# Performance work log

Hardware: AMD Instinct MI355X
Metric: run time of the kernel (lower is better)

## Reference

```python
import jax, jax.numpy as jnp
import numpy as np
import math

MIN_NORM = 1e-15
EPS = 4e-3  # float32 boundary eps used by PoincareBall.proj
C = 1.0


def artanh(x):
    x = jnp.clip(x, -1.0 + 1e-7, 1.0 - 1e-7)
    return 0.5 * (jnp.log1p(x) - jnp.log1p(-x))


def _norm(x):
    return jnp.maximum(jnp.linalg.norm(x, axis=-1, keepdims=True), MIN_NORM)


def proj(x, c):
    n = _norm(x)
    maxnorm = (1.0 - EPS) / jnp.sqrt(c)
    return jnp.where(n > maxnorm, x / n * maxnorm, x)


def expmap0(u, c):
    sc = jnp.sqrt(c)
    n = _norm(u)
    return jnp.tanh(sc * n) * u / (sc * n)


def logmap0(p, c):
    sc = jnp.sqrt(c)
    n = _norm(p)
    return artanh(sc * n) * p / (sc * n)


def mobius_add(x, y, c):
    x2 = jnp.sum(x * x, -1, keepdims=True)
    y2 = jnp.sum(y * y, -1, keepdims=True)
    xy = jnp.sum(x * y, -1, keepdims=True)
    num = (1 + 2 * c * xy + c * y2) * x + (1 - c * x2) * y
    den = 1 + 2 * c * xy + c * c * x2 * y2
    return num / jnp.maximum(den, MIN_NORM)


def mobius_matvec(m, x, c):
    sc = jnp.sqrt(c)
    xn = _norm(x)
    mx = x @ m.T
    mxn = _norm(mx)
    res = jnp.tanh(mxn / xn * artanh(sc * xn)) * mx / (mxn * sc)
    zero = jnp.all(mx == 0, axis=-1, keepdims=True)
    return jnp.where(zero, jnp.zeros((), x.dtype), res)


def hnn_layer(x, W, b, c):
    # HypLinear (dropout=0, use_bias=1) followed by HypAct(relu); proj_tan0 is identity for PoincareBall.
    res = proj(mobius_matvec(W, x, c), c)
    hb = proj(expmap0(b.reshape(1, -1), c), c)
    res = proj(mobius_add(res, hb, c), c)
    xt = jax.nn.relu(logmap0(res, c))
    return proj(expmap0(xt, c), c)


def setup_inputs():
    key = jax.random.key(0)
    ks = jax.random.split(key, 5)
    B, N, K, D = 4, 2000, 5, 32
    H1, H2 = 160, 32  # H_layer1: 32 -> 32*5, H_layer2: 32 -> 32
    # points on the Poincare ball (small norm so logmap0 is well-conditioned)
    in_feats = 0.05 * jax.random.normal(ks[0], (B, N, D), jnp.float32)
    # one-hot neighbor adjacency [batch, agent, nei, agent]
    nei_idx = jax.random.randint(ks[1], (B, N, K), 0, N)
    in_nei = jax.nn.one_hot(nei_idx, N, dtype=jnp.float32)
    # xavier_uniform with gain sqrt(2), zero bias (reset_parameters)
    b1w = math.sqrt(2.0) * math.sqrt(6.0 / (H1 + D))
    b2w = math.sqrt(2.0) * math.sqrt(6.0 / (H2 + H2))
    W1 = jax.random.uniform(ks[2], (H1, D), jnp.float32, -b1w, b1w)
    W2 = jax.random.uniform(ks[3], (H2, H2), jnp.float32, -b2w, b2w)
    b1 = jnp.zeros((H1,), jnp.float32)
    b2 = jnp.zeros((H2,), jnp.float32)
    return {"in_feats": in_feats, "in_nei": in_nei, "W1": W1, "b1": b1,
            "W2": W2, "b2": b2, "h_dim": 32, "head": 5}


def reference(in_feats, in_nei, W1, b1, W2, b2, h_dim, head):
    c = C
    B, N, D = in_feats.shape
    K = in_nei.shape[2]
    # tangent-space features (proj_tan0 is identity)
    feats = logmap0(in_feats, c)                                   # [B,N,D]
    agent = proj(expmap0(feats[:, :, None, :], c), c)              # [B,N,1,D]
    # one-hot adjacency gather: equals matmul(in_nei, repeat(feats)) in the torch code
    nbr_t = jnp.einsum('bnkm,bmd->bnkd', in_nei, feats)            # [B,N,K,D]
    nbr = proj(expmap0(nbr_t, c), c)
    # query heads
    q = logmap0(hnn_layer(agent, W1, b1, c), c)                    # [B,N,1,h*head]
    q = q.reshape(B, N, 1, h_dim, head).transpose(0, 1, 4, 2, 3)   # [B,N,head,1,h]
    # key heads; the torch code recomputes H_layer1(neighbor_repr) for values with
    # identical weights/inputs (dropout=0), so values == keys and we reuse them.
    kv = logmap0(hnn_layer(nbr, W1, b1, c), c)
    kv = kv.reshape(B, N, K, h_dim, head).transpose(0, 1, 4, 2, 3)  # [B,N,head,K,h]
    att = jax.nn.softmax(jnp.einsum('bnhqd,bnhkd->bnhqk', q, kv), axis=-1)  # [B,N,head,1,K]
    att_record = att.reshape(B, N, head, K)
    out = jnp.einsum('bnhqk,bnhkd->bnhqd', att, kv).mean(axis=2)   # [B,N,1,h]
    out = out.reshape(B, N, h_dim)
    out = proj(expmap0(out, c), c)
    out = hnn_layer(out, W2, b2, c)                                # [B,N,32]
    return out, att_record
```

## Files before the change

kernel.cpp:

```cpp
#include <hip/hip_runtime.h>
#include <math.h>

#define BB 4
#define NN 2000
#define KK 5
#define DD 32
#define H1 160
#define HEAD 5
#define HDIM 32
#define MAXNORM 0.996f
#define MINN 1e-15f

#define NIDX_BLOCKS 10000
#define NG_BLOCKS 2000

__device__ __forceinline__ float artanh_f(float x) {
    x = fminf(fmaxf(x, -1.0f + 1e-7f), 1.0f - 1e-7f);
    return 0.5f * (log1pf(x) - log1pf(-x));
}

__device__ __forceinline__ float wave_sum(float v) {
#pragma unroll
    for (int o = 32; o > 0; o >>= 1) v += __shfl_xor(v, o, 64);
    return v;
}

__device__ __forceinline__ float wave_sum32(float v) {
#pragma unroll
    for (int o = 16; o > 0; o >>= 1) v += __shfl_xor(v, o, 64);
    return v;
}

__device__ __forceinline__ void do_find_idx(const float* __restrict__ nei,
                                            int* __restrict__ idx,
                                            int wave, int lane) {
    const float* row = nei + (size_t)wave * NN;
#pragma unroll 1
    for (int it = 0; it < 8; ++it) {
        int base = it * 256 + lane * 4;
        bool found = false;
        int pos = 0;
        if (base < NN) {
            float4 v = *(const float4*)(row + base);
            if (v.x > 0.5f) { found = true; pos = base; }
            if (v.y > 0.5f) { found = true; pos = base + 1; }
            if (v.z > 0.5f) { found = true; pos = base + 2; }
            if (v.w > 0.5f) { found = true; pos = base + 3; }
        }
        unsigned long long m = __ballot(found);
        if (m) {
            if (found) idx[wave] = pos;
            break;
        }
    }
}

__device__ __forceinline__ void do_g(const float* __restrict__ xin,
                                     const float* __restrict__ W1,
                                     const float* __restrict__ b1,
                                     float* __restrict__ g,
                                     int wave, int lane) {
    bool j2ok = lane < (H1 - 128);

    float x = (lane < DD) ? xin[wave * DD + lane] : 0.f;

    float n = fmaxf(sqrtf(wave_sum(x * x)), MINN);
    float f = (artanh_f(n) / n) * x;
    float fn = fmaxf(sqrtf(wave_sum(f * f)), MINN);
    float p = (tanhf(fn) / fn) * f;
    float pn = fmaxf(sqrtf(wave_sum(p * p)), MINN);
    if (pn > MAXNORM) p *= MAXNORM / pn;
    float xn = fmaxf(sqrtf(wave_sum(p * p)), MINN);

    float mx0 = 0.f, mx1 = 0.f, mx2 = 0.f;
#pragma unroll
    for (int d = 0; d < DD; ++d) {
        float pd = __shfl(p, d, 64);
        mx0 += W1[lane * DD + d] * pd;
        mx1 += W1[(lane + 64) * DD + d] * pd;
        if (j2ok) mx2 += W1[(lane + 128) * DD + d] * pd;
    }
    float m2 = mx0 * mx0 + mx1 * mx1 + (j2ok ? mx2 * mx2 : 0.f);
    float mxn = fmaxf(sqrtf(wave_sum(m2)), MINN);
    float sc = tanhf(mxn / xn * artanh_f(xn)) / mxn;
    float r0 = sc * mx0, r1 = sc * mx1, r2 = sc * mx2;
    float rn = fmaxf(sqrtf(wave_sum(r0 * r0 + r1 * r1 + (j2ok ? r2 * r2 : 0.f))), MINN);
    if (rn > MAXNORM) { float s = MAXNORM / rn; r0 *= s; r1 *= s; r2 *= s; }

    float bb0 = b1[lane], bb1 = b1[lane + 64], bb2 = j2ok ? b1[lane + 128] : 0.f;
    float bn = fmaxf(sqrtf(wave_sum(bb0 * bb0 + bb1 * bb1 + bb2 * bb2)), MINN);
    float bs = tanhf(bn) / bn;
    float h0 = bs * bb0, h1 = bs * bb1, h2 = bs * bb2;
    float hn = fmaxf(sqrtf(wave_sum(h0 * h0 + h1 * h1 + h2 * h2)), MINN);
    if (hn > MAXNORM) { float s = MAXNORM / hn; h0 *= s; h1 *= s; h2 *= s; }

    float x2s = wave_sum(r0 * r0 + r1 * r1 + (j2ok ? r2 * r2 : 0.f));
    float y2s = wave_sum(h0 * h0 + h1 * h1 + h2 * h2);
    float xys = wave_sum(r0 * h0 + r1 * h1 + (j2ok ? r2 * h2 : 0.f));
    float ca = 1.f + 2.f * xys + y2s;
    float cb = 1.f - x2s;
    float den = fmaxf(1.f + 2.f * xys + x2s * y2s, MINN);
    float a0 = (ca * r0 + cb * h0) / den;
    float a1 = (ca * r1 + cb * h1) / den;
    float a2 = (ca * r2 + cb * h2) / den;
    float an = fmaxf(sqrtf(wave_sum(a0 * a0 + a1 * a1 + (j2ok ? a2 * a2 : 0.f))), MINN);
    if (an > MAXNORM) { float s = MAXNORM / an; a0 *= s; a1 *= s; a2 *= s; }

    float ln = fmaxf(sqrtf(wave_sum(a0 * a0 + a1 * a1 + (j2ok ? a2 * a2 : 0.f))), MINN);
    float ls = artanh_f(ln) / ln;
    float t0 = fmaxf(ls * a0, 0.f), t1 = fmaxf(ls * a1, 0.f), t2 = fmaxf(ls * a2, 0.f);
    float tn = fmaxf(sqrtf(wave_sum(t0 * t0 + t1 * t1 + (j2ok ? t2 * t2 : 0.f))), MINN);
    float es = tanhf(tn) / tn;
    float y0 = es * t0, y1 = es * t1, y2 = es * t2;
    float yn = fmaxf(sqrtf(wave_sum(y0 * y0 + y1 * y1 + (j2ok ? y2 * y2 : 0.f))), MINN);
    if (yn > MAXNORM) { float s = MAXNORM / yn; y0 *= s; y1 *= s; y2 *= s; }
    float gn = fmaxf(sqrtf(wave_sum(y0 * y0 + y1 * y1 + (j2ok ? y2 * y2 : 0.f))), MINN);
    float gs = artanh_f(gn) / gn;

    float* go = g + (size_t)wave * H1;
    go[lane] = gs * y0;
    go[lane + 64] = gs * y1;
    if (j2ok) go[lane + 128] = gs * y2;
}

__global__ __launch_bounds__(256) void scan_and_g_kernel(const float* __restrict__ nei,
                                                         int* __restrict__ idx,
                                                         const float* __restrict__ xin,
                                                         const float* __restrict__ W1,
                                                         const float* __restrict__ b1,
                                                         float* __restrict__ g) {
    int lane = threadIdx.x & 63;
    int waveInBlock = threadIdx.x >> 6;
    if (blockIdx.x < NIDX_BLOCKS) {
        int wave = blockIdx.x * 4 + waveInBlock;
        do_find_idx(nei, idx, wave, lane);
    } else {
        int wave = (blockIdx.x - NIDX_BLOCKS) * 4 + waveInBlock;
        do_g(xin, W1, b1, g, wave, lane);
    }
}

__global__ __launch_bounds__(256) void fused_att_out_kernel(const float* __restrict__ g,
                                                            const int* __restrict__ idx,
                                                            const float* __restrict__ W2,
                                                            const float* __restrict__ b2,
                                                            float* __restrict__ out,
                                                            float* __restrict__ att_out) {
    int wave = (blockIdx.x * blockDim.x + threadIdx.x) >> 6;
    int lane = threadIdx.x & 63;
    if (wave >= BB * NN) return;
    int r = wave;
    int b = r / NN;
    int d = lane & 31;

    const float* gq = g + (size_t)r * H1;
    float q[HEAD];
#pragma unroll
    for (int h = 0; h < HEAD; ++h) q[h] = gq[d * HEAD + h];

    float kv[KK][HEAD];
    float s[KK][HEAD];
#pragma unroll
    for (int k = 0; k < KK; ++k) {
        int m = idx[r * KK + k];
        const float* gk = g + (size_t)(b * NN + m) * H1;
#pragma unroll
        for (int h = 0; h < HEAD; ++h) kv[k][h] = gk[d * HEAD + h];
#pragma unroll
        for (int h = 0; h < HEAD; ++h) s[k][h] = wave_sum32(q[h] * kv[k][h]);
    }

    float att[HEAD][KK];
#pragma unroll
    for (int h = 0; h < HEAD; ++h) {
        float mxv = s[0][h];
#pragma unroll
        for (int k = 1; k < KK; ++k) mxv = fmaxf(mxv, s[k][h]);
        float sum = 0.f;
#pragma unroll
        for (int k = 0; k < KK; ++k) { att[h][k] = expf(s[k][h] - mxv); sum += att[h][k]; }
        float inv = 1.f / sum;
#pragma unroll
        for (int k = 0; k < KK; ++k) att[h][k] *= inv;
    }
    if (lane < HEAD * KK) {
        int h = lane / KK, k = lane % KK;
        att_out[(size_t)r * HEAD * KK + lane] = att[h][k];
    }

    float o = 0.f;
#pragma unroll
    for (int h = 0; h < HEAD; ++h)
#pragma unroll
        for (int k = 0; k < KK; ++k) o += att[h][k] * kv[k][h];
    o *= (1.f / HEAD);

    float n = fmaxf(sqrtf(wave_sum32(o * o)), MINN);
    o *= tanhf(n) / n;
    n = fmaxf(sqrtf(wave_sum32(o * o)), MINN);
    if (n > MAXNORM) o *= MAXNORM / n;

    float xn = fmaxf(sqrtf(wave_sum32(o * o)), MINN);
    float mx = 0.f;
#pragma unroll
    for (int dd = 0; dd < HDIM; ++dd) {
        float od = __shfl(o, dd, 64);
        mx += W2[d * HDIM + dd] * od;
    }
    float mxn = fmaxf(sqrtf(wave_sum32(mx * mx)), MINN);
    float sc = tanhf(mxn / xn * artanh_f(xn)) / mxn;
    mx *= sc;
    float rn = fmaxf(sqrtf(wave_sum32(mx * mx)), MINN);
    if (rn > MAXNORM) mx *= MAXNORM / rn;

    float hb = b2[d];
    float bn = fmaxf(sqrtf(wave_sum32(hb * hb)), MINN);
    hb *= tanhf(bn) / bn;
    float hn = fmaxf(sqrtf(wave_sum32(hb * hb)), MINN);
    if (hn > MAXNORM) hb *= MAXNORM / hn;

    float x2s = wave_sum32(mx * mx);
    float y2s = wave_sum32(hb * hb);
    float xys = wave_sum32(mx * hb);
    float ca = 1.f + 2.f * xys + y2s;
    float cb = 1.f - x2s;
    float den = fmaxf(1.f + 2.f * xys + x2s * y2s, MINN);
    float a = (ca * mx + cb * hb) / den;
    float an = fmaxf(sqrtf(wave_sum32(a * a)), MINN);
    if (an > MAXNORM) a *= MAXNORM / an;

    float ln = fmaxf(sqrtf(wave_sum32(a * a)), MINN);
    a = fmaxf((artanh_f(ln) / ln) * a, 0.f);
    float tn = fmaxf(sqrtf(wave_sum32(a * a)), MINN);
    a *= tanhf(tn) / tn;
    float yn = fmaxf(sqrtf(wave_sum32(a * a)), MINN);
    if (yn > MAXNORM) a *= MAXNORM / yn;

    if (lane < HDIM) out[(size_t)r * HDIM + lane] = a;
}

extern "C" void kernel_launch(void* const* d_in, const int* in_sizes, int n_in,
                              void* d_out, int out_size, void* d_ws, size_t ws_size,
                              hipStream_t stream) {
    const float* in_feats = (const float*)d_in[0];
    const float* in_nei = (const float*)d_in[1];
    const float* W1 = (const float*)d_in[2];
    const float* b1 = (const float*)d_in[3];
    const float* W2 = (const float*)d_in[4];
    const float* b2 = (const float*)d_in[5];

    int* idx = (int*)d_ws;
    size_t idx_bytes = ((size_t)BB * NN * KK * sizeof(int) + 255) & ~(size_t)255;
    float* g = (float*)((char*)d_ws + idx_bytes);

    float* out = (float*)d_out;
    float* att = out + (size_t)BB * NN * HDIM;

    hipLaunchKernelGGL(scan_and_g_kernel, dim3(NIDX_BLOCKS + NG_BLOCKS), dim3(256), 0, stream,
                       in_nei, idx, in_feats, W1, b1, g);
    hipLaunchKernelGGL(fused_att_out_kernel, dim3((BB * NN * 64 + 255) / 256), dim3(256), 0, stream,
                       g, idx, W2, b2, out, att);
}
```

Baseline: 516.4 us.

## Replace redundant norm reductions with analytic norms, interleave blocks, nontemporal scan loads

Norms after expmap, projection and logmap are now computed analytically from the tanh/artanh values instead of through fresh wave reductions. This removes many shuffle-reduction chains in both kernels. The scan kernel interleaves index-scan blocks with feature blocks in a 5:1 pattern, uses nontemporal loads for the one-hot adjacency stream, and gets occupancy hints in launch_bounds. The attention kernel issues all neighbor gathers before the dot products. Replacing recomputed norms with analytic ones can shift rounding slightly.

```diff
diff --git a/kernel.cpp b/kernel.cpp
--- a/kernel.cpp
+++ b/kernel.cpp
@@ -11,8 +11,9 @@
 #define MAXNORM 0.996f
 #define MINN 1e-15f
 
-#define NIDX_BLOCKS 10000
-#define NG_BLOCKS 2000
+#define TOTAL_BLOCKS 12000
+
+typedef float vfloat4 __attribute__((ext_vector_type(4)));
 
 __device__ __forceinline__ float artanh_f(float x) {
     x = fminf(fmaxf(x, -1.0f + 1e-7f), 1.0f - 1e-7f);
@@ -41,11 +42,11 @@
         bool found = false;
         int pos = 0;
         if (base < NN) {
-            float4 v = *(const float4*)(row + base);
-            if (v.x > 0.5f) { found = true; pos = base; }
-            if (v.y > 0.5f) { found = true; pos = base + 1; }
-            if (v.z > 0.5f) { found = true; pos = base + 2; }
-            if (v.w > 0.5f) { found = true; pos = base + 3; }
+            vfloat4 v = __builtin_nontemporal_load((const vfloat4*)(row + base));
+            if (v[0] > 0.5f) { found = true; pos = base; }
+            if (v[1] > 0.5f) { found = true; pos = base + 1; }
+            if (v[2] > 0.5f) { found = true; pos = base + 2; }
+            if (v[3] > 0.5f) { found = true; pos = base + 3; }
         }
         unsigned long long m = __ballot(found);
         if (m) {
@@ -65,12 +66,14 @@
     float x = (lane < DD) ? xin[wave * DD + lane] : 0.f;
 
     float n = fmaxf(sqrtf(wave_sum(x * x)), MINN);
-    float f = (artanh_f(n) / n) * x;
-    float fn = fmaxf(sqrtf(wave_sum(f * f)), MINN);
-    float p = (tanhf(fn) / fn) * f;
-    float pn = fmaxf(sqrtf(wave_sum(p * p)), MINN);
+    float fa = artanh_f(n);
+    float f = (fa / n) * x;
+    float fn = fmaxf(fa, MINN);
+    float tp = tanhf(fn);
+    float p = (tp / fn) * f;
+    float pn = tp;
     if (pn > MAXNORM) p *= MAXNORM / pn;
-    float xn = fmaxf(sqrtf(wave_sum(p * p)), MINN);
+    float xn = fmaxf(fminf(pn, MAXNORM), MINN);
 
     float mx0 = 0.f, mx1 = 0.f, mx2 = 0.f;
 #pragma unroll
@@ -82,20 +85,24 @@
     }
     float m2 = mx0 * mx0 + mx1 * mx1 + (j2ok ? mx2 * mx2 : 0.f);
     float mxn = fmaxf(sqrtf(wave_sum(m2)), MINN);
-    float sc = tanhf(mxn / xn * artanh_f(xn)) / mxn;
+    float tr = tanhf(mxn / xn * artanh_f(xn));
+    float sc = tr / mxn;
     float r0 = sc * mx0, r1 = sc * mx1, r2 = sc * mx2;
-    float rn = fmaxf(sqrtf(wave_sum(r0 * r0 + r1 * r1 + (j2ok ? r2 * r2 : 0.f))), MINN);
+    float rn = tr;
     if (rn > MAXNORM) { float s = MAXNORM / rn; r0 *= s; r1 *= s; r2 *= s; }
+    rn = fminf(rn, MAXNORM);
 
     float bb0 = b1[lane], bb1 = b1[lane + 64], bb2 = j2ok ? b1[lane + 128] : 0.f;
     float bn = fmaxf(sqrtf(wave_sum(bb0 * bb0 + bb1 * bb1 + bb2 * bb2)), MINN);
-    float bs = tanhf(bn) / bn;
+    float tb = tanhf(bn);
+    float bs = tb / bn;
     float h0 = bs * bb0, h1 = bs * bb1, h2 = bs * bb2;
-    float hn = fmaxf(sqrtf(wave_sum(h0 * h0 + h1 * h1 + h2 * h2)), MINN);
+    float hn = tb;
     if (hn > MAXNORM) { float s = MAXNORM / hn; h0 *= s; h1 *= s; h2 *= s; }
-
-    float x2s = wave_sum(r0 * r0 + r1 * r1 + (j2ok ? r2 * r2 : 0.f));
-    float y2s = wave_sum(h0 * h0 + h1 * h1 + h2 * h2);
+    hn = fminf(hn, MAXNORM);
+
+    float x2s = rn * rn;
+    float y2s = hn * hn;
     float xys = wave_sum(r0 * h0 + r1 * h1 + (j2ok ? r2 * h2 : 0.f));
     float ca = 1.f + 2.f * xys + y2s;
     float cb = 1.f - x2s;
@@ -105,17 +112,19 @@
     float a2 = (ca * r2 + cb * h2) / den;
     float an = fmaxf(sqrtf(wave_sum(a0 * a0 + a1 * a1 + (j2ok ? a2 * a2 : 0.f))), MINN);
     if (an > MAXNORM) { float s = MAXNORM / an; a0 *= s; a1 *= s; a2 *= s; }
-
-    float ln = fmaxf(sqrtf(wave_sum(a0 * a0 + a1 * a1 + (j2ok ? a2 * a2 : 0.f))), MINN);
-    float ls = artanh_f(ln) / ln;
+    float an2 = fmaxf(fminf(an, MAXNORM), MINN);
+
+    float ls = artanh_f(an2) / an2;
     float t0 = fmaxf(ls * a0, 0.f), t1 = fmaxf(ls * a1, 0.f), t2 = fmaxf(ls * a2, 0.f);
     float tn = fmaxf(sqrtf(wave_sum(t0 * t0 + t1 * t1 + (j2ok ? t2 * t2 : 0.f))), MINN);
-    float es = tanhf(tn) / tn;
+    float te = tanhf(tn);
+    float es = te / tn;
     float y0 = es * t0, y1 = es * t1, y2 = es * t2;
-    float yn = fmaxf(sqrtf(wave_sum(y0 * y0 + y1 * y1 + (j2ok ? y2 * y2 : 0.f))), MINN);
-    if (yn > MAXNORM) { float s = MAXNORM / yn; y0 *= s; y1 *= s; y2 *= s; }
-    float gn = fmaxf(sqrtf(wave_sum(y0 * y0 + y1 * y1 + (j2ok ? y2 * y2 : 0.f))), MINN);
-    float gs = artanh_f(gn) / gn;
+    float yn = te;
+    float s2 = (yn > MAXNORM) ? (MAXNORM / yn) : 1.f;
+    y0 *= s2; y1 *= s2; y2 *= s2;
+    float yn2 = fmaxf(fminf(yn, MAXNORM), MINN);
+    float gs = artanh_f(yn2) / yn2;
 
     float* go = g + (size_t)wave * H1;
     go[lane] = gs * y0;
@@ -123,29 +132,32 @@
     if (j2ok) go[lane + 128] = gs * y2;
 }
 
-__global__ __launch_bounds__(256) void scan_and_g_kernel(const float* __restrict__ nei,
-                                                         int* __restrict__ idx,
-                                                         const float* __restrict__ xin,
-                                                         const float* __restrict__ W1,
-                                                         const float* __restrict__ b1,
-                                                         float* __restrict__ g) {
+__global__ __launch_bounds__(256, 8) void scan_and_g_kernel(const float* __restrict__ nei,
+                                                            int* __restrict__ idx,
+                                                            const float* __restrict__ xin,
+                                                            const float* __restrict__ W1,
+                                                            const float* __restrict__ b1,
+                                                            float* __restrict__ g) {
     int lane = threadIdx.x & 63;
     int waveInBlock = threadIdx.x >> 6;
-    if (blockIdx.x < NIDX_BLOCKS) {
-        int wave = blockIdx.x * 4 + waveInBlock;
+    unsigned bi = blockIdx.x;
+    unsigned q6 = bi / 6u;
+    unsigned r6 = bi - q6 * 6u;
+    if (r6 == 5u) {
+        int wave = (int)q6 * 4 + waveInBlock;
+        do_g(xin, W1, b1, g, wave, lane);
+    } else {
+        int wave = (int)(q6 * 5u + r6) * 4 + waveInBlock;
         do_find_idx(nei, idx, wave, lane);
-    } else {
-        int wave = (blockIdx.x - NIDX_BLOCKS) * 4 + waveInBlock;
-        do_g(xin, W1, b1, g, wave, lane);
-    }
-}
-
-__global__ __launch_bounds__(256) void fused_att_out_kernel(const float* __restrict__ g,
-                                                            const int* __restrict__ idx,
-                                                            const float* __restrict__ W2,
-                                                            const float* __restrict__ b2,
-                                                            float* __restrict__ out,
-                                                            float* __restrict__ att_out) {
+    }
+}
+
+__global__ __launch_bounds__(256, 4) void fused_att_out_kernel(const float* __restrict__ g,
+                                                               const int* __restrict__ idx,
+                                                               const float* __restrict__ W2,
+                                                               const float* __restrict__ b2,
+                                                               float* __restrict__ out,
+                                                               float* __restrict__ att_out) {
     int wave = (blockIdx.x * blockDim.x + threadIdx.x) >> 6;
     int lane = threadIdx.x & 63;
     if (wave >= BB * NN) return;
@@ -158,17 +170,21 @@
 #pragma unroll
     for (int h = 0; h < HEAD; ++h) q[h] = gq[d * HEAD + h];
 
+    int nb[KK];
+#pragma unroll
+    for (int k = 0; k < KK; ++k) nb[k] = idx[r * KK + k];
     float kv[KK][HEAD];
+#pragma unroll
+    for (int k = 0; k < KK; ++k) {
+        const float* gk = g + (size_t)(b * NN + nb[k]) * H1 + d * HEAD;
+#pragma unroll
+        for (int h = 0; h < HEAD; ++h) kv[k][h] = gk[h];
+    }
     float s[KK][HEAD];
 #pragma unroll
-    for (int k = 0; k < KK; ++k) {
-        int m = idx[r * KK + k];
-        const float* gk = g + (size_t)(b * NN + m) * H1;
-#pragma unroll
-        for (int h = 0; h < HEAD; ++h) kv[k][h] = gk[d * HEAD + h];
+    for (int k = 0; k < KK; ++k)
 #pragma unroll
         for (int h = 0; h < HEAD; ++h) s[k][h] = wave_sum32(q[h] * kv[k][h]);
-    }
 
     float att[HEAD][KK];
 #pragma unroll
@@ -196,11 +212,12 @@
     o *= (1.f / HEAD);
 
     float n = fmaxf(sqrtf(wave_sum32(o * o)), MINN);
-    o *= tanhf(n) / n;
-    n = fmaxf(sqrtf(wave_sum32(o * o)), MINN);
-    if (n > MAXNORM) o *= MAXNORM / n;
-
-    float xn = fmaxf(sqrtf(wave_sum32(o * o)), MINN);
+    float to = tanhf(n);
+    o *= to / n;
+    float on = to;
+    if (on > MAXNORM) o *= MAXNORM / on;
+    float xn = fmaxf(fminf(on, MAXNORM), MINN);
+
     float mx = 0.f;
 #pragma unroll
     for (int dd = 0; dd < HDIM; ++dd) {
@@ -208,19 +225,22 @@
         mx += W2[d * HDIM + dd] * od;
     }
     float mxn = fmaxf(sqrtf(wave_sum32(mx * mx)), MINN);
-    float sc = tanhf(mxn / xn * artanh_f(xn)) / mxn;
-    mx *= sc;
-    float rn = fmaxf(sqrtf(wave_sum32(mx * mx)), MINN);
+    float tr = tanhf(mxn / xn * artanh_f(xn));
+    mx *= tr / mxn;
+    float rn = tr;
     if (rn > MAXNORM) mx *= MAXNORM / rn;
+    rn = fminf(rn, MAXNORM);
 
     float hb = b2[d];
     float bn = fmaxf(sqrtf(wave_sum32(hb * hb)), MINN);
-    hb *= tanhf(bn) / bn;
-    float hn = fmaxf(sqrtf(wave_sum32(hb * hb)), MINN);
+    float tb = tanhf(bn);
+    hb *= tb / bn;
+    float hn = tb;
     if (hn > MAXNORM) hb *= MAXNORM / hn;
-
-    float x2s = wave_sum32(mx * mx);
-    float y2s = wave_sum32(hb * hb);
+    hn = fminf(hn, MAXNORM);
+
+    float x2s = rn * rn;
+    float y2s = hn * hn;
     float xys = wave_sum32(mx * hb);
     float ca = 1.f + 2.f * xys + y2s;
     float cb = 1.f - x2s;
@@ -228,12 +248,13 @@
     float a = (ca * mx + cb * hb) / den;
     float an = fmaxf(sqrtf(wave_sum32(a * a)), MINN);
     if (an > MAXNORM) a *= MAXNORM / an;
-
-    float ln = fmaxf(sqrtf(wave_sum32(a * a)), MINN);
-    a = fmaxf((artanh_f(ln) / ln) * a, 0.f);
+    float an2 = fmaxf(fminf(an, MAXNORM), MINN);
+
+    a = fmaxf((artanh_f(an2) / an2) * a, 0.f);
     float tn = fmaxf(sqrtf(wave_sum32(a * a)), MINN);
-    a *= tanhf(tn) / tn;
-    float yn = fmaxf(sqrtf(wave_sum32(a * a)), MINN);
+    float te = tanhf(tn);
+    a *= te / tn;
+    float yn = te;
     if (yn > MAXNORM) a *= MAXNORM / yn;
 
     if (lane < HDIM) out[(size_t)r * HDIM + lane] = a;
@@ -256,7 +277,7 @@
     float* out = (float*)d_out;
     float* att = out + (size_t)BB * NN * HDIM;
 
-    hipLaunchKernelGGL(scan_and_g_kernel, dim3(NIDX_BLOCKS + NG_BLOCKS), dim3(256), 0, stream,
+    hipLaunchKernelGGL(scan_and_g_kernel, dim3(TOTAL_BLOCKS), dim3(256), 0, stream,
                        in_nei, idx, in_feats, W1, b1, g);
     hipLaunchKernelGGL(fused_att_out_kernel, dim3((BB * NN * 64 + 255) / 256), dim3(256), 0, stream,
                        g, idx, W2, b2, out, att);
```

After: 600.5 us. +16.3%, slower.
